# Kernel tuning notes

Hardware: AMD Instinct MI355X
Metric: run time of the kernel (lower is better)

Reference implementation:

```python
import jax, jax.numpy as jnp
import numpy as np
from jax import lax

HIDDEN = 256
WIDTH = 1024
DEPTH = 4
T = 64
SUBSTEPS = 8  # fixed RK4 substeps per save interval (replaces diffrax adaptive Tsit5)

Y0 = np.array([0.0008417, 0.01495894, 0.00082556, 0.00068982, 0.00063456,
               0.00832867, 0.00190631, 0.00155624, 0.00142264, 0.01858621,
               0.02000239, 0.01796071, 0.01670121, 0.22218046, 0.02531468,
               0.03337227, 0.6147068], dtype=np.float32)


def setup_inputs() -> dict:
    key = jax.random.key(0)
    ks = jax.random.split(key, 8)

    def lin(k, out, inp):
        kw, kb = jax.random.split(k)
        lim = 1.0 / np.sqrt(inp)
        W = jax.random.uniform(kw, (out, inp), jnp.float32, -lim, lim)
        b = jax.random.uniform(kb, (out,), jnp.float32, -lim, lim)
        return W, b

    W0, b0 = lin(ks[0], WIDTH, HIDDEN + 17)
    Whs, bhs = [], []
    for i in range(DEPTH - 1):
        w, b = lin(ks[1 + i], WIDTH, WIDTH)
        Whs.append(w)
        bhs.append(b)
    Wh = jnp.stack(Whs)   # [DEPTH-1, WIDTH, WIDTH]
    bh = jnp.stack(bhs)   # [DEPTH-1, WIDTH]
    Wl, bl = lin(ks[4], HIDDEN, WIDTH)
    beta_W, beta_b = lin(ks[5], 1, HIDDEN)
    hvec = 0.01 * jax.random.normal(ks[6], (HIDDEN,), jnp.float32)
    scale = jnp.array([0.1], jnp.float32)
    y0_log = jnp.log(jnp.asarray(Y0))
    ts = jnp.arange(T, dtype=jnp.float32) * 0.25  # save points (months)
    return dict(ts=ts, W0=W0, b0=b0, Wh=Wh, bh=bh, Wl=Wl, bl=bl,
                beta_W=beta_W, beta_b=beta_b, hvec=hvec, scale=scale,
                y0_log=y0_log)


def _forward(ts, W0, b0, Wh, bh, Wl, bl, beta_W, beta_b, hvec, scale, y0_log):
    xi, mu, sigma, nu, gamma = 13/12, 0.041/12, 91/12, 36/12, 1.8/12

    def mlp(x):  # softplus hidden activations, final tanh(0.01*x)
        z = jax.nn.softplus(W0 @ x + b0)
        def body(z, wb):
            w, b = wb
            return jax.nn.softplus(w @ z + b), None
        z, _ = lax.scan(body, z, (Wh, bh))
        return jnp.tanh(0.01 * (Wl @ z + bl))

    def rhs(y):  # y = concat(state[17], h[HIDDEN])
        state, h = y[:17], y[17:]
        bb1 = 8.0 * jax.nn.sigmoid(beta_W @ h + beta_b)[0] + 25.0
        bb2, bb3, bb4 = 0.5 * bb1, 0.35 * bb1, 0.25 * bb1
        M, S1, E1, E2, E3, E4, I1, I2, I3, I4, R1, R2, R3, R4, S2, S3, S4 = state
        I = I1 + I2 + I3 + I4
        R = R1 + R2 + R3 + R4
        dstate = jnp.stack([
            R * mu - (xi + mu) * M,
            mu * (1 - R) + xi * M - mu * S1 - bb1 * I * S1,
            bb1 * I * S1 - (mu + sigma) * E1,
            bb2 * I * S2 - (mu + sigma) * E2,
            bb3 * I * S3 - (mu + sigma) * E3,
            bb4 * I * S4 - (mu + sigma) * E4,
            sigma * E1 - (nu + mu) * I1,
            sigma * E2 - (nu + mu) * I2,
            sigma * E3 - (nu + mu) * I3,
            sigma * E4 - (nu + mu) * I4,
            nu * I1 - (mu + gamma) * R1,
            nu * I2 - (mu + gamma) * R2,
            nu * I3 - (mu + gamma) * R3,
            nu * I4 - (mu + gamma) * R4,
            gamma * R1 - mu * S2 - bb2 * I * S2,
            gamma * R2 - mu * S3 - bb3 * I * S3,
            gamma * (R3 + R4) - mu * S4 - bb4 * I * S4,
        ])
        dh = scale[0] * mlp(jnp.concatenate([h, state]))
        return jnp.concatenate([dstate, dh])

    def rk4(y, dt):
        k1 = rhs(y)
        k2 = rhs(y + 0.5 * dt * k1)
        k3 = rhs(y + 0.5 * dt * k2)
        k4 = rhs(y + dt * k3)
        return y + (dt / 6.0) * (k1 + 2 * k2 + 2 * k3 + k4)

    y0 = jnp.concatenate([jax.nn.softmax(y0_log), hvec])

    def interval(y, dt_i):
        dt = dt_i / SUBSTEPS
        def step(y, _):
            return rk4(y, dt), None
        y, _ = lax.scan(step, y, None, length=SUBSTEPS)
        return y, y

    dts = ts[1:] - ts[:-1]
    _, ys = lax.scan(interval, y0, dts)
    ys = jnp.concatenate([y0[None], ys], axis=0)  # [T, 17+HIDDEN]
    return ys[:, :17], ys[:, 17:]


def reference(ts, W0, b0, Wh, bh, Wl, bl, beta_W, beta_b, hvec, scale, y0_log):
    return _forward(ts, W0, b0, Wh, bh, Wl, bl, beta_W, beta_b, hvec, scale, y0_log)
```

## Files before the change

kernel.cpp:

```cpp
#include <hip/hip_runtime.h>
#include <math.h>

#define NBLK    32
#define NLAUNCH 256
#define BS      512
#define NSTATE  17
#define NH      256
#define NX      273
#define WID     1024
#define NT      64
#define NSUB    8
#define ROWS_H  (WID/NBLK)
#define ROWS_L  (NH/NBLK)
#define POLL_CAP 2000000

typedef unsigned long long u64;
typedef unsigned int u32;

__device__ __forceinline__ float softplus_f(float v) {
    return fmaxf(v, 0.f) + log1pf(expf(-fabsf(v)));
}

__device__ __forceinline__ u32 bf16_rne(float x) {
    u32 u = __float_as_uint(x);
    return (u + 0x7FFFu + ((u >> 16) & 1u)) >> 16;
}
__device__ __forceinline__ void st_pack(u64* p, float ve, float vo, unsigned tag) {
    u32 lo = (bf16_rne(ve) << 16) | bf16_rne(vo);
    u64 w = ((u64)(tag ^ lo) << 32) | (u64)lo;
    asm volatile("global_atomic_swap_x2 %0, %1, off" :: "v"(p), "v"(w) : "memory");
}
__device__ __forceinline__ void st_tag(u64* p, float v, unsigned tag) {
    u32 lo = __float_as_uint(v);
    u64 w = ((u64)(tag ^ lo) << 32) | (u64)lo;
    asm volatile("global_atomic_swap_x2 %0, %1, off" :: "v"(p), "v"(w) : "memory");
}
__device__ __forceinline__ u64 ld_tag(const u64* p) {
    u64 w;
    asm volatile("global_atomic_add_x2 %0, %1, %2, off sc0\n\t"
                 "s_waitcnt vmcnt(0)"
                 : "=&v"(w) : "v"(p), "v"(0ULL) : "memory");
    return w;
}
__device__ __forceinline__ bool tag_ok(u64 w, unsigned tag) {
    return (((u32)(w >> 32)) ^ ((u32)w)) == tag;
}

__device__ __forceinline__ void consume_z(const u64* __restrict__ buf,
                                          unsigned tag,
                                          float* __restrict__ z_s, int t) {
    __syncthreads();
    const u64* p = buf + t;
    u64 w; int it = 0;
    do { w = ld_tag(p); } while (!tag_ok(w, tag) && ++it < POLL_CAP);
    u32 lo = (u32)w;
    z_s[2 * t]     = __uint_as_float(lo & 0xFFFF0000u);
    z_s[2 * t + 1] = __uint_as_float(lo << 16);
    __syncthreads();
}

extern "C" __global__ __launch_bounds__(BS, 2) void ode_kernel(
    const float* __restrict__ ts,   const float* __restrict__ W0,
    const float* __restrict__ b0,   const float* __restrict__ Wh,
    const float* __restrict__ bh,   const float* __restrict__ Wl,
    const float* __restrict__ bl,   const float* __restrict__ betaW,
    const float* __restrict__ betab,const float* __restrict__ hvec,
    const float* __restrict__ scale,const float* __restrict__ y0log,
    float* __restrict__ out, u64* zA64, u64* zB64, u64* dh64, unsigned* ctrl)
{
    const int t = threadIdx.x;

    __shared__ int      role_sh;
    __shared__ unsigned tagbase_sh;
    __shared__ float y_s[NX];
    __shared__ float yn_s[NX];
    __shared__ float xm[NX];
    __shared__ float k_s[NX];
    __shared__ float z_s[WID];
    __shared__ float red[8];
    __shared__ float dt_sh;
    extern __shared__ float wh2[];

    if (t == 0) {
        int xcd;
        asm volatile("s_getreg_b32 %0, hwreg(HW_REG_XCC_ID)" : "=s"(xcd));
        xcd &= 7;
        unsigned rk = atomicAdd(&ctrl[xcd], 1u);
        if (rk == NBLK - 1) {
            u64 rt;
            asm volatile("s_memrealtime %0\n\ts_waitcnt lgkmcnt(0)" : "=s"(rt));
            unsigned word = (((unsigned)(rt >> 4)) << 4) | (unsigned)(xcd + 1);
            atomicCAS(&ctrl[8], 0u, word);
        }
        unsigned w; int it = 0;
        do {
            w = __hip_atomic_load(&ctrl[8], __ATOMIC_RELAXED, __HIP_MEMORY_SCOPE_AGENT);
        } while (w == 0u && ++it < POLL_CAP);
        role_sh    = (w != 0u && xcd == (int)(w & 0xFu) - 1 && rk < NBLK) ? (int)rk : -1;
        tagbase_sh = w;
    }
    __syncthreads();
    const int blk = role_sh;
    const unsigned tagbase = tagbase_sh;
    if (blk < 0) return;

    const float scale0 = scale[0];
    const float betab0 = betab[0];
    unsigned R = 0;

    const int rowH = t >> 4, laneH = t & 15;
    const int growH = blk * ROWS_H + rowH;
    const int rowL = t >> 6, laneL = t & 63;
    const int growL = blk * ROWS_L + rowL;

    const int packIdx = blk * (ROWS_H / 2) + (rowH >> 1);

    const float b0r = b0[growH];
    float bhr[3];
    bhr[0] = bh[growH]; bhr[1] = bh[WID + growH]; bhr[2] = bh[2 * WID + growH];
    const float blr    = bl[growL];
    const float betaWr = (t < NH) ? betaW[t] : 0.f;
    const float* wlp = Wl + (size_t)growL * WID + laneL * 4;

    float4 wv0[16], wv1[16];
    {
        const float* whp = Wh + (size_t)growH * WID + laneH * 4;
        #pragma unroll
        for (int i = 0; i < 16; i++) wv0[i] = *(const float4*)(whp + i * 64);
        #pragma unroll
        for (int i = 0; i < 16; i++) wv1[i] = *(const float4*)(whp + WID * WID + i * 64);
    }
    {
        const float* src = Wh + 2 * (size_t)WID * WID + (size_t)blk * ROWS_H * WID;
        for (int i = t * 4; i < ROWS_H * WID; i += BS * 4)
            *(float4*)&wh2[i] = *(const float4*)&src[i];
    }
    float w0r[18];
    {
        const float* w0p = W0 + (size_t)growH * NX;
        #pragma unroll
        for (int i = 0; i < 18; i++) {
            int c = laneH + i * 16;
            w0r[i] = (c < NX) ? w0p[c] : 0.f;
        }
    }

    if (t < NSTATE) {
        float m = -1e30f;
        for (int j = 0; j < NSTATE; j++) m = fmaxf(m, y0log[j]);
        float ssum = 0.f;
        for (int j = 0; j < NSTATE; j++) ssum += expf(y0log[j] - m);
        y_s[t] = expf(y0log[t] - m) / ssum;
    }
    if (t < NH) y_s[NSTATE + t] = hvec[t];
    __syncthreads();

    if (blk == 0) {
        if (t < NSTATE) out[t] = y_s[t];
        if (t < NH)     out[NT * NSTATE + t] = y_s[NSTATE + t];
    }

    const float c_xi = 13.f / 12.f, c_mu = 0.041f / 12.f, c_sig = 91.f / 12.f,
                c_nu = 36.f / 12.f, c_gam = 1.8f / 12.f;

    for (int iv = 0; iv < NT - 1; iv++) {
        if (t == 0) dt_sh = (ts[iv + 1] - ts[iv]) * (1.f / NSUB);
        __syncthreads();
        const float dt = dt_sh;

        for (int sub = 0; sub < NSUB; sub++) {
            if (t < NX) yn_s[t] = y_s[t];

            for (int s = 0; s < 4; s++) {
                const float a   = (s == 0) ? 0.f : ((s == 3) ? 1.f : 0.5f);
                const float wgt = ((s == 0) || (s == 3)) ? dt * (1.f / 6.f) : dt * (1.f / 3.f);
                const float adt = a * dt;

                if (t < NX) {
                    const int src = (t < NH) ? (NSTATE + t) : (t - NH);
                    float v = y_s[src];
                    if (s != 0) v = fmaf(adt, k_s[src], v);
                    xm[t] = v;
                }
                __syncthreads();

                {
                    float acc = 0.f;
                    #pragma unroll
                    for (int i = 0; i < 18; i++) {
                        int c = laneH + i * 16;
                        if (c < NX) acc = fmaf(w0r[i], xm[c], acc);
                    }
                    #pragma unroll
                    for (int m = 1; m < 16; m <<= 1) acc += __shfl_xor(acc, m, 16);
                    float val = softplus_f(acc + b0r);
                    float vodd = __shfl(val, (t & 63) + 16, 64);
                    ++R;
                    if ((t & 31) == 0) st_pack(&zA64[packIdx], val, vodd, tagbase + R);
                }

                {
                    if (t < NH) {
                        float p = betaWr * xm[t];
                        #pragma unroll
                        for (int m = 1; m < 64; m <<= 1) p += __shfl_xor(p, m, 64);
                        if ((t & 63) == 0) red[t >> 6] = p;
                    }
                    __syncthreads();
                    if (t == 0) {
                        const float* xs = xm + NH;
                        float sd  = red[0] + red[1] + red[2] + red[3] + betab0;
                        float bb1 = 8.f / (1.f + expf(-sd)) + 25.f;
                        float bb2 = 0.5f * bb1, bb3 = 0.35f * bb1, bb4 = 0.25f * bb1;
                        float M  = xs[0],  S1 = xs[1],  E1 = xs[2],  E2 = xs[3];
                        float E3 = xs[4],  E4 = xs[5],  I1 = xs[6],  I2 = xs[7];
                        float I3 = xs[8],  I4 = xs[9],  R1 = xs[10], R2 = xs[11];
                        float R3 = xs[12], R4 = xs[13], S2 = xs[14], S3 = xs[15];
                        float S4 = xs[16];
                        float I = I1 + I2 + I3 + I4, Rs = R1 + R2 + R3 + R4;
                        k_s[0]  = Rs * c_mu - (c_xi + c_mu) * M;
                        k_s[1]  = c_mu * (1.f - Rs) + c_xi * M - c_mu * S1 - bb1 * I * S1;
                        k_s[2]  = bb1 * I * S1 - (c_mu + c_sig) * E1;
                        k_s[3]  = bb2 * I * S2 - (c_mu + c_sig) * E2;
                        k_s[4]  = bb3 * I * S3 - (c_mu + c_sig) * E3;
                        k_s[5]  = bb4 * I * S4 - (c_mu + c_sig) * E4;
                        k_s[6]  = c_sig * E1 - (c_nu + c_mu) * I1;
                        k_s[7]  = c_sig * E2 - (c_nu + c_mu) * I2;
                        k_s[8]  = c_sig * E3 - (c_nu + c_mu) * I3;
                        k_s[9]  = c_sig * E4 - (c_nu + c_mu) * I4;
                        k_s[10] = c_nu * I1 - (c_mu + c_gam) * R1;
                        k_s[11] = c_nu * I2 - (c_mu + c_gam) * R2;
                        k_s[12] = c_nu * I3 - (c_mu + c_gam) * R3;
                        k_s[13] = c_nu * I4 - (c_mu + c_gam) * R4;
                        k_s[14] = c_gam * R1 - c_mu * S2 - bb2 * I * S2;
                        k_s[15] = c_gam * R2 - c_mu * S3 - bb3 * I * S3;
                        k_s[16] = c_gam * (R3 + R4) - c_mu * S4 - bb4 * I * S4;
                    }
                }

                auto hidden = [&](const float4 (&wv)[16], const u64* zin64,
                                  u64* zout64, float bias) {
                    consume_z(zin64, tagbase + R, z_s, t);
                    float acc = 0.f;
                    #pragma unroll
                    for (int i = 0; i < 16; i++) {
                        float4 zv = *(const float4*)(z_s + (laneH * 4 + i * 64));
                        acc = fmaf(wv[i].x, zv.x, acc);
                        acc = fmaf(wv[i].y, zv.y, acc);
                        acc = fmaf(wv[i].z, zv.z, acc);
                        acc = fmaf(wv[i].w, zv.w, acc);
                    }
                    #pragma unroll
                    for (int m = 1; m < 16; m <<= 1) acc += __shfl_xor(acc, m, 16);
                    float val = softplus_f(acc + bias);
                    float vodd = __shfl(val, (t & 63) + 16, 64);
                    ++R;
                    if ((t & 31) == 0) st_pack(&zout64[packIdx], val, vodd, tagbase + R);
                };

                hidden(wv0, zA64, zB64, bhr[0]);
                hidden(wv1, zB64, zA64, bhr[1]);

                float4 wvL[4];
                #pragma unroll
                for (int i = 0; i < 4; i++) wvL[i] = *(const float4*)(wlp + i * 256);

                {
                    consume_z(zA64, tagbase + R, z_s, t);
                    const float* wr = wh2 + rowH * WID + laneH * 4;
                    float acc = 0.f;
                    #pragma unroll
                    for (int i = 0; i < 16; i++) {
                        float4 wv4 = *(const float4*)(wr + i * 64);
                        float4 zv  = *(const float4*)(z_s + (laneH * 4 + i * 64));
                        acc = fmaf(wv4.x, zv.x, acc);
                        acc = fmaf(wv4.y, zv.y, acc);
                        acc = fmaf(wv4.z, zv.z, acc);
                        acc = fmaf(wv4.w, zv.w, acc);
                    }
                    #pragma unroll
                    for (int m = 1; m < 16; m <<= 1) acc += __shfl_xor(acc, m, 16);
                    float val = softplus_f(acc + bhr[2]);
                    float vodd = __shfl(val, (t & 63) + 16, 64);
                    ++R;
                    if ((t & 31) == 0) st_pack(&zB64[packIdx], val, vodd, tagbase + R);
                }

                {
                    consume_z(zB64, tagbase + R, z_s, t);
                    float acc = 0.f;
                    #pragma unroll
                    for (int i = 0; i < 4; i++) {
                        float4 zv = *(const float4*)(z_s + (laneL * 4 + i * 256));
                        acc = fmaf(wvL[i].x, zv.x, acc);
                        acc = fmaf(wvL[i].y, zv.y, acc);
                        acc = fmaf(wvL[i].z, zv.z, acc);
                        acc = fmaf(wvL[i].w, zv.w, acc);
                    }
                    #pragma unroll
                    for (int m = 1; m < 64; m <<= 1) acc += __shfl_xor(acc, m, 64);
                    ++R;
                    if (laneL == 0)
                        st_tag(&dh64[growL], scale0 * tanhf(0.01f * (acc + blr)), tagbase + R);
                }

                {
                    if (t < NH) {
                        u64 w; int it = 0;
                        do { w = ld_tag(dh64 + t); }
                        while (!tag_ok(w, tagbase + R) && ++it < POLL_CAP);
                        k_s[NSTATE + t] = __uint_as_float((u32)w);
                    }
                    __syncthreads();
                    if (t < NX) yn_s[t] = fmaf(wgt, k_s[t], yn_s[t]);
                }
            }

            __syncthreads();
            if (t < NX) y_s[t] = yn_s[t];
            __syncthreads();
        }

        if (blk == 0) {
            if (t < NSTATE) out[(iv + 1) * NSTATE + t] = y_s[t];
            if (t < NH)     out[NT * NSTATE + (iv + 1) * NH + t] = y_s[NSTATE + t];
        }
    }
}

extern "C" void kernel_launch(void* const* d_in, const int* in_sizes, int n_in,
                              void* d_out, int out_size, void* d_ws, size_t ws_size,
                              hipStream_t stream) {
    const float* ts    = (const float*)d_in[0];
    const float* W0    = (const float*)d_in[1];
    const float* b0    = (const float*)d_in[2];
    const float* Wh    = (const float*)d_in[3];
    const float* bh    = (const float*)d_in[4];
    const float* Wl    = (const float*)d_in[5];
    const float* bl    = (const float*)d_in[6];
    const float* betaW = (const float*)d_in[7];
    const float* betab = (const float*)d_in[8];
    const float* hvec  = (const float*)d_in[9];
    const float* scale = (const float*)d_in[10];
    const float* y0log = (const float*)d_in[11];
    float* out = (float*)d_out;

    u64*      zA64 = (u64*)d_ws;
    u64*      zB64 = (u64*)((char*)d_ws + 4096);
    u64*      dh64 = (u64*)((char*)d_ws + 8192);
    unsigned* ctrl = (unsigned*)((char*)d_ws + 10240);

    static int lds_set = 0;
    if (!lds_set) {
        hipFuncSetAttribute((const void*)ode_kernel,
                            hipFuncAttributeMaxDynamicSharedMemorySize, 131072);
        lds_set = 1;
    }

    hipMemsetAsync(d_ws, 0, 10240 + 64, stream);
    hipLaunchKernelGGL(ode_kernel, dim3(NLAUNCH), dim3(BS), 131072, stream,
                       ts, W0, b0, Wh, bh, Wl, bl, betaW, betab, hvec, scale,
                       y0log, out, zA64, zB64, dh64, ctrl);
}
```

Baseline: 22.80 ms.

## Replace per-element tag polling with per-block sentinel flags and plain loads

Each producer block now drains its stores and publishes a single tagged sentinel per stage. Consumers poll only the 32 block sentinels, invalidate the cache, and then read the data with ordinary loads, falling back to atomic polling if a tag mismatches. This is meant to cut the many atomic-polling loads every thread issued per layer. The SEIR scalar computation also moves to thread 256 after the fence so it overlaps with other work. In exchange, each stage gains an extra vmcnt wait, a block barrier and a cache invalidate.

```diff
diff --git a/kernel.cpp b/kernel.cpp
--- a/kernel.cpp
+++ b/kernel.cpp
@@ -46,13 +46,32 @@
     return (((u32)(w >> 32)) ^ ((u32)w)) == tag;
 }
 
+#define SENT_STRIDE 16
+
+__device__ __forceinline__ void publish_fence(u64* sent, int blk, unsigned tag, int t) {
+    asm volatile("s_waitcnt vmcnt(0)" ::: "memory");
+    __syncthreads();
+    if (t == 0) st_tag(sent + blk * SENT_STRIDE, 0.f, tag);
+}
+__device__ __forceinline__ void wait_sent(const u64* sent, unsigned tag, int t) {
+    if (t < NBLK) {
+        const u64* sp = sent + t * SENT_STRIDE;
+        u64 w; int it = 0;
+        do { w = ld_tag(sp); } while (!tag_ok(w, tag) && ++it < POLL_CAP);
+    }
+    __syncthreads();
+    asm volatile("buffer_inv" ::: "memory");
+}
 __device__ __forceinline__ void consume_z(const u64* __restrict__ buf,
+                                          const u64* __restrict__ sent,
                                           unsigned tag,
                                           float* __restrict__ z_s, int t) {
-    __syncthreads();
-    const u64* p = buf + t;
-    u64 w; int it = 0;
-    do { w = ld_tag(p); } while (!tag_ok(w, tag) && ++it < POLL_CAP);
+    wait_sent(sent, tag, t);
+    u64 w = buf[t];
+    if (!tag_ok(w, tag)) {
+        int it = 0;
+        do { w = ld_tag(buf + t); } while (!tag_ok(w, tag) && ++it < POLL_CAP);
+    }
     u32 lo = (u32)w;
     z_s[2 * t]     = __uint_as_float(lo & 0xFFFF0000u);
     z_s[2 * t + 1] = __uint_as_float(lo << 16);
@@ -66,7 +85,8 @@
     const float* __restrict__ bl,   const float* __restrict__ betaW,
     const float* __restrict__ betab,const float* __restrict__ hvec,
     const float* __restrict__ scale,const float* __restrict__ y0log,
-    float* __restrict__ out, u64* zA64, u64* zB64, u64* dh64, unsigned* ctrl)
+    float* __restrict__ out, u64* zA64, u64* zB64, u64* dh64,
+    u64* sent, unsigned* ctrl)
 {
     const int t = threadIdx.x;
 
@@ -199,48 +219,47 @@
                     if ((t & 31) == 0) st_pack(&zA64[packIdx], val, vodd, tagbase + R);
                 }
 
-                {
-                    if (t < NH) {
-                        float p = betaWr * xm[t];
-                        #pragma unroll
-                        for (int m = 1; m < 64; m <<= 1) p += __shfl_xor(p, m, 64);
-                        if ((t & 63) == 0) red[t >> 6] = p;
-                    }
-                    __syncthreads();
-                    if (t == 0) {
-                        const float* xs = xm + NH;
-                        float sd  = red[0] + red[1] + red[2] + red[3] + betab0;
-                        float bb1 = 8.f / (1.f + expf(-sd)) + 25.f;
-                        float bb2 = 0.5f * bb1, bb3 = 0.35f * bb1, bb4 = 0.25f * bb1;
-                        float M  = xs[0],  S1 = xs[1],  E1 = xs[2],  E2 = xs[3];
-                        float E3 = xs[4],  E4 = xs[5],  I1 = xs[6],  I2 = xs[7];
-                        float I3 = xs[8],  I4 = xs[9],  R1 = xs[10], R2 = xs[11];
-                        float R3 = xs[12], R4 = xs[13], S2 = xs[14], S3 = xs[15];
-                        float S4 = xs[16];
-                        float I = I1 + I2 + I3 + I4, Rs = R1 + R2 + R3 + R4;
-                        k_s[0]  = Rs * c_mu - (c_xi + c_mu) * M;
-                        k_s[1]  = c_mu * (1.f - Rs) + c_xi * M - c_mu * S1 - bb1 * I * S1;
-                        k_s[2]  = bb1 * I * S1 - (c_mu + c_sig) * E1;
-                        k_s[3]  = bb2 * I * S2 - (c_mu + c_sig) * E2;
-                        k_s[4]  = bb3 * I * S3 - (c_mu + c_sig) * E3;
-                        k_s[5]  = bb4 * I * S4 - (c_mu + c_sig) * E4;
-                        k_s[6]  = c_sig * E1 - (c_nu + c_mu) * I1;
-                        k_s[7]  = c_sig * E2 - (c_nu + c_mu) * I2;
-                        k_s[8]  = c_sig * E3 - (c_nu + c_mu) * I3;
-                        k_s[9]  = c_sig * E4 - (c_nu + c_mu) * I4;
-                        k_s[10] = c_nu * I1 - (c_mu + c_gam) * R1;
-                        k_s[11] = c_nu * I2 - (c_mu + c_gam) * R2;
-                        k_s[12] = c_nu * I3 - (c_mu + c_gam) * R3;
-                        k_s[13] = c_nu * I4 - (c_mu + c_gam) * R4;
-                        k_s[14] = c_gam * R1 - c_mu * S2 - bb2 * I * S2;
-                        k_s[15] = c_gam * R2 - c_mu * S3 - bb3 * I * S3;
-                        k_s[16] = c_gam * (R3 + R4) - c_mu * S4 - bb4 * I * S4;
-                    }
+                if (t < NH) {
+                    float p = betaWr * xm[t];
+                    #pragma unroll
+                    for (int m = 1; m < 64; m <<= 1) p += __shfl_xor(p, m, 64);
+                    if ((t & 63) == 0) red[t >> 6] = p;
+                }
+                publish_fence(sent, blk, tagbase + R, t);
+
+                if (t == 256) {
+                    const float* xs = xm + NH;
+                    float sd  = red[0] + red[1] + red[2] + red[3] + betab0;
+                    float bb1 = 8.f / (1.f + expf(-sd)) + 25.f;
+                    float bb2 = 0.5f * bb1, bb3 = 0.35f * bb1, bb4 = 0.25f * bb1;
+                    float M  = xs[0],  S1 = xs[1],  E1 = xs[2],  E2 = xs[3];
+                    float E3 = xs[4],  E4 = xs[5],  I1 = xs[6],  I2 = xs[7];
+                    float I3 = xs[8],  I4 = xs[9],  R1 = xs[10], R2 = xs[11];
+                    float R3 = xs[12], R4 = xs[13], S2 = xs[14], S3 = xs[15];
+                    float S4 = xs[16];
+                    float I = I1 + I2 + I3 + I4, Rs = R1 + R2 + R3 + R4;
+                    k_s[0]  = Rs * c_mu - (c_xi + c_mu) * M;
+                    k_s[1]  = c_mu * (1.f - Rs) + c_xi * M - c_mu * S1 - bb1 * I * S1;
+                    k_s[2]  = bb1 * I * S1 - (c_mu + c_sig) * E1;
+                    k_s[3]  = bb2 * I * S2 - (c_mu + c_sig) * E2;
+                    k_s[4]  = bb3 * I * S3 - (c_mu + c_sig) * E3;
+                    k_s[5]  = bb4 * I * S4 - (c_mu + c_sig) * E4;
+                    k_s[6]  = c_sig * E1 - (c_nu + c_mu) * I1;
+                    k_s[7]  = c_sig * E2 - (c_nu + c_mu) * I2;
+                    k_s[8]  = c_sig * E3 - (c_nu + c_mu) * I3;
+                    k_s[9]  = c_sig * E4 - (c_nu + c_mu) * I4;
+                    k_s[10] = c_nu * I1 - (c_mu + c_gam) * R1;
+                    k_s[11] = c_nu * I2 - (c_mu + c_gam) * R2;
+                    k_s[12] = c_nu * I3 - (c_mu + c_gam) * R3;
+                    k_s[13] = c_nu * I4 - (c_mu + c_gam) * R4;
+                    k_s[14] = c_gam * R1 - c_mu * S2 - bb2 * I * S2;
+                    k_s[15] = c_gam * R2 - c_mu * S3 - bb3 * I * S3;
+                    k_s[16] = c_gam * (R3 + R4) - c_mu * S4 - bb4 * I * S4;
                 }
 
                 auto hidden = [&](const float4 (&wv)[16], const u64* zin64,
                                   u64* zout64, float bias) {
-                    consume_z(zin64, tagbase + R, z_s, t);
+                    consume_z(zin64, sent, tagbase + R, z_s, t);
                     float acc = 0.f;
                     #pragma unroll
                     for (int i = 0; i < 16; i++) {
@@ -256,6 +275,7 @@
                     float vodd = __shfl(val, (t & 63) + 16, 64);
                     ++R;
                     if ((t & 31) == 0) st_pack(&zout64[packIdx], val, vodd, tagbase + R);
+                    publish_fence(sent, blk, tagbase + R, t);
                 };
 
                 hidden(wv0, zA64, zB64, bhr[0]);
@@ -266,7 +286,7 @@
                 for (int i = 0; i < 4; i++) wvL[i] = *(const float4*)(wlp + i * 256);
 
                 {
-                    consume_z(zA64, tagbase + R, z_s, t);
+                    consume_z(zA64, sent, tagbase + R, z_s, t);
                     const float* wr = wh2 + rowH * WID + laneH * 4;
                     float acc = 0.f;
                     #pragma unroll
@@ -284,10 +304,11 @@
                     float vodd = __shfl(val, (t & 63) + 16, 64);
                     ++R;
                     if ((t & 31) == 0) st_pack(&zB64[packIdx], val, vodd, tagbase + R);
+                    publish_fence(sent, blk, tagbase + R, t);
                 }
 
                 {
-                    consume_z(zB64, tagbase + R, z_s, t);
+                    consume_z(zB64, sent, tagbase + R, z_s, t);
                     float acc = 0.f;
                     #pragma unroll
                     for (int i = 0; i < 4; i++) {
@@ -302,13 +323,18 @@
                     ++R;
                     if (laneL == 0)
                         st_tag(&dh64[growL], scale0 * tanhf(0.01f * (acc + blr)), tagbase + R);
+                    publish_fence(sent, blk, tagbase + R, t);
                 }
 
                 {
+                    wait_sent(sent, tagbase + R, t);
                     if (t < NH) {
-                        u64 w; int it = 0;
-                        do { w = ld_tag(dh64 + t); }
-                        while (!tag_ok(w, tagbase + R) && ++it < POLL_CAP);
+                        u64 w = dh64[t];
+                        if (!tag_ok(w, tagbase + R)) {
+                            int it = 0;
+                            do { w = ld_tag(dh64 + t); }
+                            while (!tag_ok(w, tagbase + R) && ++it < POLL_CAP);
+                        }
                         k_s[NSTATE + t] = __uint_as_float((u32)w);
                     }
                     __syncthreads();
@@ -348,7 +374,8 @@
     u64*      zA64 = (u64*)d_ws;
     u64*      zB64 = (u64*)((char*)d_ws + 4096);
     u64*      dh64 = (u64*)((char*)d_ws + 8192);
-    unsigned* ctrl = (unsigned*)((char*)d_ws + 10240);
+    u64*      sent = (u64*)((char*)d_ws + 10240);
+    unsigned* ctrl = (unsigned*)((char*)d_ws + 14336);
 
     static int lds_set = 0;
     if (!lds_set) {
@@ -357,8 +384,8 @@
         lds_set = 1;
     }
 
-    hipMemsetAsync(d_ws, 0, 10240 + 64, stream);
+    hipMemsetAsync(d_ws, 0, 14336 + 64, stream);
     hipLaunchKernelGGL(ode_kernel, dim3(NLAUNCH), dim3(BS), 131072, stream,
                        ts, W0, b0, Wh, bh, Wl, bl, betaW, betab, hvec, scale,
-                       y0log, out, zA64, zB64, dh64, ctrl);
-}
+                       y0log, out, zA64, zB64, dh64, sent, ctrl);
+}
```

After: 25.54 ms. +12.0%, slower.
